# Kernel optimization log

Measured on AMD Instinct MI355X. Metric: run time of the kernel, lower is better.

## Reference

```python
import jax, jax.numpy as jnp
import numpy as np

B, C, H, W = 16, 256, 64, 64
C8, C2 = C // 8, C // 2


def conv1x1(x, w, b):
    # x: [B,Cin,H,W], w: [Cout,Cin], b: [Cout]
    return jnp.einsum('oc,bchw->bohw', w, x) + b[None, :, None, None]


def maxpool2(x):
    # 2x2 max pool, stride 2. x: [B,C,H,W] -> [B,C,H//2,W//2]
    b, c, h, w = x.shape
    return x.reshape(b, c, h // 2, 2, w // 2, 2).max(axis=(3, 5))


def setup_inputs() -> dict:
    key = jax.random.key(0)
    ks = jax.random.split(key, 9)
    s = lambda fan_in: 1.0 / np.sqrt(fan_in)
    return {
        'x': jax.random.normal(ks[0], (B, C, H, W), jnp.float32),
        'w_theta': jax.random.normal(ks[1], (C8, C), jnp.float32) * s(C),
        'b_theta': jax.random.normal(ks[2], (C8,), jnp.float32) * 0.01,
        'w_phi': jax.random.normal(ks[3], (C8, C), jnp.float32) * s(C),
        'b_phi': jax.random.normal(ks[4], (C8,), jnp.float32) * 0.01,
        'w_g': jax.random.normal(ks[5], (C2, C), jnp.float32) * s(C),
        'b_g': jax.random.normal(ks[6], (C2,), jnp.float32) * 0.01,
        'w_o': jax.random.normal(ks[7], (C, C2), jnp.float32) * s(C2),
        'b_o': jax.random.normal(ks[8], (C,), jnp.float32) * 0.01,
        'gamma': jnp.full((1,), 0.5, jnp.float32),
    }


def reference(x, w_theta, b_theta, w_phi, b_phi, w_g, b_g, w_o, b_o, gamma):
    b, c, h, w = x.shape
    n, m = h * w, (h * w) // 4
    theta = conv1x1(x, w_theta, b_theta).reshape(b, C8, n)        # [B,C/8,N]
    phi = maxpool2(conv1x1(x, w_phi, b_phi)).reshape(b, C8, m)    # [B,C/8,M]
    g = maxpool2(conv1x1(x, w_g, b_g)).reshape(b, C2, m)          # [B,C/2,M]
    # beta = softmax(theta^T phi) over keys M
    scores = jnp.einsum('bcn,bcm->bnm', theta, phi)               # [B,N,M]
    beta = jax.nn.softmax(scores, axis=-1)
    o_pre = jnp.einsum('bcm,bnm->bcn', g, beta).reshape(b, C2, h, w)
    o = conv1x1(o_pre, w_o, b_o)                                  # [B,C,H,W]
    return gamma[0] * o + x
```

## Files before the change

kernel.cpp:

```cpp
#include <hip/hip_runtime.h>
#include <hip/hip_bf16.h>

#define BB 16
#define NN 4096
#define MM 1024

typedef __attribute__((ext_vector_type(8))) short bf16x8;
typedef __attribute__((ext_vector_type(4))) float f32x4;

__device__ __forceinline__ unsigned short f2bfbits(float f) {
    union { float f; unsigned u; } v; v.f = f;
    unsigned r = v.u + 0x7fffu + ((v.u >> 16) & 1u);
    return (unsigned short)(r >> 16);
}
__device__ __forceinline__ float bfraw(unsigned short u) {
    union { unsigned u; float f; } v; v.u = ((unsigned)u) << 16; return v.f;
}

__global__ void prep_kernel(
    const float* __restrict__ wt, const float* __restrict__ bt,
    const float* __restrict__ wp, const float* __restrict__ bp,
    const float* __restrict__ wg, const float* __restrict__ bg,
    const float* __restrict__ wo,
    unsigned short* __restrict__ w_all, unsigned short* __restrict__ w_o_bf,
    float* __restrict__ b_all)
{
    int i = blockIdx.x * 256 + threadIdx.x;
    if (i < 8192)        w_all[i] = f2bfbits(wt[i]);
    else if (i < 16384)  w_all[i] = f2bfbits(wp[i - 8192]);
    else if (i < 49152)  w_all[i] = f2bfbits(wg[i - 16384]);
    else if (i < 81920)  w_o_bf[i - 49152] = f2bfbits(wo[i - 49152]);
    else if (i < 82112) {
        int r = i - 81920;
        b_all[r] = (r < 32) ? bt[r] : (r < 64) ? bp[r - 32] : bg[r - 64];
    }
}

__global__ __launch_bounds__(256, 2) void proj_kernel(
    const float* __restrict__ x,
    const unsigned short* __restrict__ w_all,
    const float* __restrict__ b_all,
    unsigned short* __restrict__ theta_t,
    unsigned short* __restrict__ phi_t,
    unsigned short* __restrict__ g)
{
    __shared__ unsigned short ot[192 * 136];

    const int t = threadIdx.x;
    const int w = t >> 6;
    const int l = t & 63;
    const int lr = l & 15, lg = l >> 4;
    const int b  = blockIdx.x >> 5;
    const int pt = blockIdx.x & 31;
    const int pbase = pt << 7;
    const int mb = pt << 5;

    f32x4 acc[3][8];
    #pragma unroll
    for (int i = 0; i < 3; ++i)
        #pragma unroll
        for (int nt = 0; nt < 8; ++nt) acc[i][nt] = (f32x4){0.f,0.f,0.f,0.f};

    const float* xb = x + (size_t)b * 256 * 4096 + pbase + lr;

    #pragma unroll 1
    for (int ks = 0; ks < 8; ++ks) {
        bf16x8 af[3];
        #pragma unroll
        for (int i = 0; i < 3; ++i)
            af[i] = *(const bf16x8*)(w_all + (size_t)(16*(3*w+i) + lr)*256 + 32*ks + 8*lg);
        #pragma unroll
        for (int nt = 0; nt < 8; ++nt) {
            const float* xp = xb + 16*nt + (size_t)(32*ks + 8*lg) * 4096;
            union { bf16x8 v; unsigned short u[8]; } bx;
            #pragma unroll
            for (int j = 0; j < 8; ++j) bx.u[j] = f2bfbits(xp[(size_t)j * 4096]);
            #pragma unroll
            for (int i = 0; i < 3; ++i)
                acc[i][nt] = __builtin_amdgcn_mfma_f32_16x16x32_bf16(af[i], bx.v, acc[i][nt], 0, 0, 0);
        }
    }

    float bias[3][4];
    #pragma unroll
    for (int i = 0; i < 3; ++i)
        #pragma unroll
        for (int r = 0; r < 4; ++r) bias[i][r] = b_all[16*(3*w+i) + 4*lg + r];
    #pragma unroll
    for (int i = 0; i < 3; ++i)
        #pragma unroll
        for (int nt = 0; nt < 8; ++nt)
            #pragma unroll
            for (int r = 0; r < 4; ++r)
                ot[(16*(3*w+i) + 4*lg + r)*136 + 16*nt + lr] =
                    f2bfbits(acc[i][nt][r] + bias[i][r]);
    __syncthreads();

    if (t < 128) {
        int p = t;
        union { unsigned short u[32]; int4 v[4]; } th;
        #pragma unroll
        for (int c = 0; c < 32; ++c) th.u[c] = ot[c*136 + p];
        int4* dst = (int4*)(theta_t + ((size_t)(b*4096 + pbase + p)) * 32);
        #pragma unroll
        for (int q = 0; q < 4; ++q) dst[q] = th.v[q];
    }
    {
        int ww = t >> 3, c0 = (t & 7) * 4;
        union { unsigned short u[4]; int2 v; } ph;
        #pragma unroll
        for (int e = 0; e < 4; ++e) {
            int row = 32 + c0 + e;
            unsigned p01 = *(const unsigned*)&ot[row*136 + 2*ww];
            unsigned p23 = *(const unsigned*)&ot[row*136 + 64 + 2*ww];
            float m0 = fmaxf(bfraw((unsigned short)p01), bfraw((unsigned short)(p01 >> 16)));
            float m1 = fmaxf(bfraw((unsigned short)p23), bfraw((unsigned short)(p23 >> 16)));
            ph.u[e] = f2bfbits(fmaxf(m0, m1));
        }
        *(int2*)(phi_t + ((size_t)(b*1024 + mb + ww)) * 32 + c0) = ph.v;
    }
    {
        int c2 = t >> 1, w0 = (t & 1) * 16;
        int row = 64 + c2;
        union { unsigned short u[16]; int4 v[2]; } gv;
        #pragma unroll
        for (int e = 0; e < 16; ++e) {
            int ww = w0 + e;
            unsigned p01 = *(const unsigned*)&ot[row*136 + 2*ww];
            unsigned p23 = *(const unsigned*)&ot[row*136 + 64 + 2*ww];
            float m0 = fmaxf(bfraw((unsigned short)p01), bfraw((unsigned short)(p01 >> 16)));
            float m1 = fmaxf(bfraw((unsigned short)p23), bfraw((unsigned short)(p23 >> 16)));
            gv.u[e] = f2bfbits(fmaxf(m0, m1));
        }
        int4* dst = (int4*)(g + ((size_t)(b*128 + c2)) * 1024 + mb + w0);
        dst[0] = gv.v[0]; dst[1] = gv.v[1];
    }
}

__global__ __launch_bounds__(64, 2) void attn_kernel(
    const unsigned short* __restrict__ theta_t,
    const unsigned short* __restrict__ phi_t,
    const unsigned short* __restrict__ g,
    unsigned short* __restrict__ o_pre_t)
{
    __shared__ unsigned short plds[32 * 72];
    __shared__ unsigned short olds[32 * 136];

    const int l = threadIdx.x;
    const int lr = l & 15, lg = l >> 4;
    const int b  = blockIdx.x >> 7;
    const int nb = (blockIdx.x & 127) << 5;

    const f32x4 zero = {0.f, 0.f, 0.f, 0.f};

    bf16x8 aq[2];
    #pragma unroll
    for (int qt = 0; qt < 2; ++qt)
        aq[qt] = *(const bf16x8*)(theta_t + ((size_t)(b*4096 + nb + 16*qt + lr))*32 + 8*lg);

    f32x4 po[2][8];
    #pragma unroll
    for (int qt = 0; qt < 2; ++qt)
        #pragma unroll
        for (int ct = 0; ct < 8; ++ct) po[qt][ct] = zero;
    float mr[2][4], lrun[2][4];
    #pragma unroll
    for (int qt = 0; qt < 2; ++qt)
        #pragma unroll
        for (int r = 0; r < 4; ++r) { mr[qt][r] = -1e30f; lrun[qt][r] = 0.f; }

    const unsigned short* phb = phi_t + (size_t)b * 1024 * 32;
    const unsigned short* gb  = g + (size_t)b * 128 * 1024;

    #pragma unroll 1
    for (int kt = 0; kt < 16; ++kt) {
        const int mb = kt * 64;
        f32x4 s[2][4];
        #pragma unroll
        for (int mt = 0; mt < 4; ++mt) {
            bf16x8 bp = *(const bf16x8*)(phb + (size_t)(mb + 16*mt + lr)*32 + 8*lg);
            s[0][mt] = __builtin_amdgcn_mfma_f32_16x16x32_bf16(aq[0], bp, zero, 0, 0, 0);
            s[1][mt] = __builtin_amdgcn_mfma_f32_16x16x32_bf16(aq[1], bp, zero, 0, 0, 0);
        }
        float sc[2][4];
        #pragma unroll
        for (int qt = 0; qt < 2; ++qt)
            #pragma unroll
            for (int r = 0; r < 4; ++r) {
                float mx = fmaxf(fmaxf(s[qt][0][r], s[qt][1][r]),
                                 fmaxf(s[qt][2][r], s[qt][3][r]));
                #pragma unroll
                for (int msk = 1; msk < 16; msk <<= 1) mx = fmaxf(mx, __shfl_xor(mx, msk));
                float nm  = fmaxf(mr[qt][r], mx);
                float scv = __expf(mr[qt][r] - nm);
                mr[qt][r] = nm; sc[qt][r] = scv;
                float ls = 0.f;
                #pragma unroll
                for (int mt = 0; mt < 4; ++mt) {
                    float p = __expf(s[qt][mt][r] - nm);
                    s[qt][mt][r] = p; ls += p;
                }
                #pragma unroll
                for (int msk = 1; msk < 16; msk <<= 1) ls += __shfl_xor(ls, msk);
                lrun[qt][r] = lrun[qt][r] * scv + ls;
            }
        #pragma unroll
        for (int qt = 0; qt < 2; ++qt)
            #pragma unroll
            for (int ct = 0; ct < 8; ++ct)
                #pragma unroll
                for (int r = 0; r < 4; ++r) po[qt][ct][r] *= sc[qt][r];
        #pragma unroll
        for (int qt = 0; qt < 2; ++qt)
            #pragma unroll
            for (int mt = 0; mt < 4; ++mt)
                #pragma unroll
                for (int r = 0; r < 4; ++r)
                    plds[(16*qt + 4*lg + r)*72 + 16*mt + lr] = f2bfbits(s[qt][mt][r]);
        #pragma unroll
        for (int ks = 0; ks < 2; ++ks) {
            bf16x8 pa0 = *(const bf16x8*)(plds + (size_t)lr*72 + 32*ks + 8*lg);
            bf16x8 pa1 = *(const bf16x8*)(plds + (size_t)(16 + lr)*72 + 32*ks + 8*lg);
            #pragma unroll
            for (int ct = 0; ct < 8; ++ct) {
                bf16x8 bg = *(const bf16x8*)(gb + (size_t)(16*ct + lr)*1024 + mb + 32*ks + 8*lg);
                po[0][ct] = __builtin_amdgcn_mfma_f32_16x16x32_bf16(pa0, bg, po[0][ct], 0, 0, 0);
                po[1][ct] = __builtin_amdgcn_mfma_f32_16x16x32_bf16(pa1, bg, po[1][ct], 0, 0, 0);
            }
        }
    }

    float inv[2][4];
    #pragma unroll
    for (int qt = 0; qt < 2; ++qt)
        #pragma unroll
        for (int r = 0; r < 4; ++r) inv[qt][r] = 1.f / lrun[qt][r];
    #pragma unroll
    for (int qt = 0; qt < 2; ++qt)
        #pragma unroll
        for (int ct = 0; ct < 8; ++ct)
            #pragma unroll
            for (int r = 0; r < 4; ++r)
                olds[(16*qt + 4*lg + r)*136 + 16*ct + lr] =
                    f2bfbits(po[qt][ct][r] * inv[qt][r]);
    #pragma unroll
    for (int i = 0; i < 8; ++i) {
        int idx = i * 64 + l;
        int q = idx >> 4, ch = idx & 15;
        int4 v = *(const int4*)(olds + q*136 + 8*ch);
        *(int4*)(o_pre_t + ((size_t)(b*4096 + nb + q))*128 + 8*ch) = v;
    }
}

__global__ __launch_bounds__(256, 2) void out_kernel(
    const unsigned short* __restrict__ o_pre_t,
    const unsigned short* __restrict__ w_o_bf,
    const float* __restrict__ b_o,
    const float* __restrict__ x,
    const float* __restrict__ gamma,
    float* __restrict__ out)
{
    const int t = threadIdx.x;
    const int w = t >> 6, l = t & 63;
    const int lr = l & 15, lg = l >> 4;
    const int b   = blockIdx.x >> 6;
    const int nbv = (blockIdx.x & 63) << 6;

    f32x4 acc[4][4];
    #pragma unroll
    for (int i = 0; i < 4; ++i)
        #pragma unroll
        for (int nt = 0; nt < 4; ++nt) acc[i][nt] = (f32x4){0.f,0.f,0.f,0.f};

    #pragma unroll 1
    for (int ks = 0; ks < 4; ++ks) {
        bf16x8 aw[4], bo[4];
        #pragma unroll
        for (int i = 0; i < 4; ++i)
            aw[i] = *(const bf16x8*)(w_o_bf + (size_t)(16*(4*w+i) + lr)*128 + 32*ks + 8*lg);
        #pragma unroll
        for (int nt = 0; nt < 4; ++nt)
            bo[nt] = *(const bf16x8*)(o_pre_t + ((size_t)(b*4096 + nbv + 16*nt + lr))*128 + 32*ks + 8*lg);
        #pragma unroll
        for (int i = 0; i < 4; ++i)
            #pragma unroll
            for (int nt = 0; nt < 4; ++nt)
                acc[i][nt] = __builtin_amdgcn_mfma_f32_16x16x32_bf16(aw[i], bo[nt], acc[i][nt], 0, 0, 0);
    }

    const float gam = gamma[0];
    float bias[4][4];
    #pragma unroll
    for (int i = 0; i < 4; ++i)
        #pragma unroll
        for (int r = 0; r < 4; ++r) bias[i][r] = b_o[16*(4*w+i) + 4*lg + r];

    #pragma unroll
    for (int i = 0; i < 4; ++i)
        #pragma unroll
        for (int nt = 0; nt < 4; ++nt)
            #pragma unroll
            for (int r = 0; r < 4; ++r) {
                int co = 16*(4*w+i) + 4*lg + r;
                int n  = nbv + 16*nt + lr;
                size_t off = ((size_t)(b*256 + co)) * 4096 + n;
                out[off] = gam * (acc[i][nt][r] + bias[i][r]) + x[off];
            }
}

extern "C" void kernel_launch(void* const* d_in, const int* in_sizes, int n_in,
                              void* d_out, int out_size, void* d_ws, size_t ws_size,
                              hipStream_t stream)
{
    const float* x       = (const float*)d_in[0];
    const float* w_theta = (const float*)d_in[1];
    const float* b_theta = (const float*)d_in[2];
    const float* w_phi   = (const float*)d_in[3];
    const float* b_phi   = (const float*)d_in[4];
    const float* w_g     = (const float*)d_in[5];
    const float* b_g     = (const float*)d_in[6];
    const float* w_o     = (const float*)d_in[7];
    const float* b_o     = (const float*)d_in[8];
    const float* gamma   = (const float*)d_in[9];
    float* outp = (float*)d_out;

    char* ws = (char*)d_ws;
    unsigned short* w_all   = (unsigned short*)ws;
    unsigned short* w_o_bf  = (unsigned short*)(ws + 98304);
    float*          b_all   = (float*)(ws + 163840);
    unsigned short* theta_t = (unsigned short*)(ws + (1u << 20));
    unsigned short* phi_t   = (unsigned short*)(ws + (5u << 20));
    unsigned short* g       = (unsigned short*)(ws + (6u << 20));
    unsigned short* o_pre_t = (unsigned short*)(ws + (10u << 20));

    prep_kernel<<<321, 256, 0, stream>>>(w_theta, b_theta, w_phi, b_phi,
                                         w_g, b_g, w_o, w_all, w_o_bf, b_all);
    proj_kernel<<<BB * 32, 256, 0, stream>>>(x, w_all, b_all, theta_t, phi_t, g);
    attn_kernel<<<BB * 128, 64, 0, stream>>>(theta_t, phi_t, g, o_pre_t);
    out_kernel<<<BB * 64, 256, 0, stream>>>(o_pre_t, w_o_bf, b_o, x, gamma, outp);
}
```

Measured before the change: 293.2 us.

## Pre-transpose x to bf16 channel-last and restructure attention to one query tile per wave

Adds a kernel that converts x to bf16 in a [B,N,C] layout so the projection kernel loads contiguous bf16x8 fragments instead of eight strided fp32 loads per fragment. The attention kernel is reorganised so each wave handles 16 queries, with 4 waves per 256-thread block. Scores are computed transposed (phi as A operand), which lets the softmax reductions use two cross-group shuffles instead of four-step butterflies. This costs an extra pass over x and more workspace, and x_t aliases o_pre_t because their lifetimes do not overlap.

```diff
diff --git a/kernel.cpp b/kernel.cpp
--- a/kernel.cpp
+++ b/kernel.cpp
@@ -2,8 +2,6 @@
 #include <hip/hip_bf16.h>
 
 #define BB 16
-#define NN 4096
-#define MM 1024
 
 typedef __attribute__((ext_vector_type(8))) short bf16x8;
 typedef __attribute__((ext_vector_type(4))) float f32x4;
@@ -15,6 +13,9 @@
 }
 __device__ __forceinline__ float bfraw(unsigned short u) {
     union { unsigned u; float f; } v; v.u = ((unsigned)u) << 16; return v.f;
+}
+__device__ __forceinline__ unsigned packbf2(float lo, float hi) {
+    return (unsigned)f2bfbits(lo) | ((unsigned)f2bfbits(hi) << 16);
 }
 
 __global__ void prep_kernel(
@@ -36,8 +37,44 @@
     }
 }
 
+__global__ __launch_bounds__(256) void xt_kernel(
+    const float* __restrict__ x, unsigned short* __restrict__ x_t)
+{
+    __shared__ unsigned short lt[64 * 74];
+
+    const int t = threadIdx.x;
+    const int bid = blockIdx.x;
+    const int b  = bid >> 8;
+    const int p0 = ((bid >> 2) & 63) << 6;
+    const int c0 = (bid & 3) << 6;
+
+    {
+        int c = t & 63, seg = t >> 6;
+        const float* src = x + ((size_t)(b * 256 + c0 + c)) * 4096 + p0 + seg * 16;
+        #pragma unroll
+        for (int j = 0; j < 4; ++j) {
+            float4 v = *(const float4*)(src + 4 * j);
+            unsigned* dst = (unsigned*)(lt + c * 74 + seg * 16 + 4 * j);
+            dst[0] = packbf2(v.x, v.y);
+            dst[1] = packbf2(v.z, v.w);
+        }
+    }
+    __syncthreads();
+    {
+        int p = t >> 2, quad = t & 3;
+        #pragma unroll
+        for (int h = 0; h < 2; ++h) {
+            union { unsigned short u[8]; int4 v; } o;
+            #pragma unroll
+            for (int e = 0; e < 8; ++e)
+                o.u[e] = lt[(quad * 16 + h * 8 + e) * 74 + p];
+            *(int4*)(x_t + ((size_t)(b * 4096 + p0 + p)) * 256 + c0 + quad * 16 + h * 8) = o.v;
+        }
+    }
+}
+
 __global__ __launch_bounds__(256, 2) void proj_kernel(
-    const float* __restrict__ x,
+    const unsigned short* __restrict__ x_t,
     const unsigned short* __restrict__ w_all,
     const float* __restrict__ b_all,
     unsigned short* __restrict__ theta_t,
@@ -61,8 +98,6 @@
         #pragma unroll
         for (int nt = 0; nt < 8; ++nt) acc[i][nt] = (f32x4){0.f,0.f,0.f,0.f};
 
-    const float* xb = x + (size_t)b * 256 * 4096 + pbase + lr;
-
     #pragma unroll 1
     for (int ks = 0; ks < 8; ++ks) {
         bf16x8 af[3];
@@ -71,13 +106,10 @@
             af[i] = *(const bf16x8*)(w_all + (size_t)(16*(3*w+i) + lr)*256 + 32*ks + 8*lg);
         #pragma unroll
         for (int nt = 0; nt < 8; ++nt) {
-            const float* xp = xb + 16*nt + (size_t)(32*ks + 8*lg) * 4096;
-            union { bf16x8 v; unsigned short u[8]; } bx;
-            #pragma unroll
-            for (int j = 0; j < 8; ++j) bx.u[j] = f2bfbits(xp[(size_t)j * 4096]);
+            bf16x8 bx = *(const bf16x8*)(x_t + ((size_t)(b*4096 + pbase + 16*nt + lr))*256 + 32*ks + 8*lg);
             #pragma unroll
             for (int i = 0; i < 3; ++i)
-                acc[i][nt] = __builtin_amdgcn_mfma_f32_16x16x32_bf16(af[i], bx.v, acc[i][nt], 0, 0, 0);
+                acc[i][nt] = __builtin_amdgcn_mfma_f32_16x16x32_bf16(af[i], bx, acc[i][nt], 0, 0, 0);
         }
     }
 
@@ -137,118 +169,104 @@
     }
 }
 
-__global__ __launch_bounds__(64, 2) void attn_kernel(
+__global__ __launch_bounds__(256, 4) void attn_kernel(
     const unsigned short* __restrict__ theta_t,
     const unsigned short* __restrict__ phi_t,
     const unsigned short* __restrict__ g,
     unsigned short* __restrict__ o_pre_t)
 {
-    __shared__ unsigned short plds[32 * 72];
-    __shared__ unsigned short olds[32 * 136];
-
-    const int l = threadIdx.x;
+    __shared__ unsigned short plds[4][16 * 72];
+    __shared__ unsigned short olds[4][16 * 136];
+
+    const int t = threadIdx.x;
+    const int wv = t >> 6;
+    const int l  = t & 63;
     const int lr = l & 15, lg = l >> 4;
-    const int b  = blockIdx.x >> 7;
-    const int nb = (blockIdx.x & 127) << 5;
+    const int b   = blockIdx.x >> 6;
+    const int nq0 = (blockIdx.x & 63) * 64 + wv * 16;
 
     const f32x4 zero = {0.f, 0.f, 0.f, 0.f};
 
-    bf16x8 aq[2];
-    #pragma unroll
-    for (int qt = 0; qt < 2; ++qt)
-        aq[qt] = *(const bf16x8*)(theta_t + ((size_t)(b*4096 + nb + 16*qt + lr))*32 + 8*lg);
-
-    f32x4 po[2][8];
-    #pragma unroll
-    for (int qt = 0; qt < 2; ++qt)
-        #pragma unroll
-        for (int ct = 0; ct < 8; ++ct) po[qt][ct] = zero;
-    float mr[2][4], lrun[2][4];
-    #pragma unroll
-    for (int qt = 0; qt < 2; ++qt)
-        #pragma unroll
-        for (int r = 0; r < 4; ++r) { mr[qt][r] = -1e30f; lrun[qt][r] = 0.f; }
+    const bf16x8 aq = *(const bf16x8*)(theta_t + ((size_t)(b*4096 + nq0 + lr))*32 + 8*lg);
+
+    f32x4 po[8];
+    #pragma unroll
+    for (int ct = 0; ct < 8; ++ct) po[ct] = zero;
+    float m_run = -1e30f, l_run = 0.f;
 
     const unsigned short* phb = phi_t + (size_t)b * 1024 * 32;
     const unsigned short* gb  = g + (size_t)b * 128 * 1024;
+    unsigned short* pw = plds[wv];
 
     #pragma unroll 1
     for (int kt = 0; kt < 16; ++kt) {
         const int mb = kt * 64;
-        f32x4 s[2][4];
+        f32x4 s[4];
         #pragma unroll
         for (int mt = 0; mt < 4; ++mt) {
-            bf16x8 bp = *(const bf16x8*)(phb + (size_t)(mb + 16*mt + lr)*32 + 8*lg);
-            s[0][mt] = __builtin_amdgcn_mfma_f32_16x16x32_bf16(aq[0], bp, zero, 0, 0, 0);
-            s[1][mt] = __builtin_amdgcn_mfma_f32_16x16x32_bf16(aq[1], bp, zero, 0, 0, 0);
-        }
-        float sc[2][4];
-        #pragma unroll
-        for (int qt = 0; qt < 2; ++qt)
+            bf16x8 ap = *(const bf16x8*)(phb + (size_t)(mb + 16*mt + lr)*32 + 8*lg);
+            s[mt] = __builtin_amdgcn_mfma_f32_16x16x32_bf16(ap, aq, zero, 0, 0, 0);
+        }
+        float mx = -1e30f;
+        #pragma unroll
+        for (int mt = 0; mt < 4; ++mt)
+            #pragma unroll
+            for (int r = 0; r < 4; ++r) mx = fmaxf(mx, s[mt][r]);
+        mx = fmaxf(mx, __shfl_xor(mx, 16));
+        mx = fmaxf(mx, __shfl_xor(mx, 32));
+        float nm = fmaxf(m_run, mx);
+        float sc = __expf(m_run - nm);
+        float ls = 0.f;
+        #pragma unroll
+        for (int mt = 0; mt < 4; ++mt)
             #pragma unroll
             for (int r = 0; r < 4; ++r) {
-                float mx = fmaxf(fmaxf(s[qt][0][r], s[qt][1][r]),
-                                 fmaxf(s[qt][2][r], s[qt][3][r]));
-                #pragma unroll
-                for (int msk = 1; msk < 16; msk <<= 1) mx = fmaxf(mx, __shfl_xor(mx, msk));
-                float nm  = fmaxf(mr[qt][r], mx);
-                float scv = __expf(mr[qt][r] - nm);
-                mr[qt][r] = nm; sc[qt][r] = scv;
-                float ls = 0.f;
-                #pragma unroll
-                for (int mt = 0; mt < 4; ++mt) {
-                    float p = __expf(s[qt][mt][r] - nm);
-                    s[qt][mt][r] = p; ls += p;
-                }
-                #pragma unroll
-                for (int msk = 1; msk < 16; msk <<= 1) ls += __shfl_xor(ls, msk);
-                lrun[qt][r] = lrun[qt][r] * scv + ls;
+                float p = __expf(s[mt][r] - nm);
+                s[mt][r] = p; ls += p;
             }
-        #pragma unroll
-        for (int qt = 0; qt < 2; ++qt)
-            #pragma unroll
-            for (int ct = 0; ct < 8; ++ct)
-                #pragma unroll
-                for (int r = 0; r < 4; ++r) po[qt][ct][r] *= sc[qt][r];
-        #pragma unroll
-        for (int qt = 0; qt < 2; ++qt)
-            #pragma unroll
-            for (int mt = 0; mt < 4; ++mt)
-                #pragma unroll
-                for (int r = 0; r < 4; ++r)
-                    plds[(16*qt + 4*lg + r)*72 + 16*mt + lr] = f2bfbits(s[qt][mt][r]);
+        ls += __shfl_xor(ls, 16);
+        ls += __shfl_xor(ls, 32);
+        l_run = l_run * sc + ls;
+        m_run = nm;
+        float scB[4];
+        #pragma unroll
+        for (int r = 0; r < 4; ++r) scB[r] = __shfl(sc, 4*lg + r);
+        #pragma unroll
+        for (int ct = 0; ct < 8; ++ct)
+            #pragma unroll
+            for (int r = 0; r < 4; ++r) po[ct][r] *= scB[r];
+        #pragma unroll
+        for (int mt = 0; mt < 4; ++mt)
+            #pragma unroll
+            for (int i = 0; i < 2; ++i)
+                *(unsigned*)(pw + lr*72 + 16*mt + 4*lg + 2*i) =
+                    packbf2(s[mt][2*i], s[mt][2*i + 1]);
         #pragma unroll
         for (int ks = 0; ks < 2; ++ks) {
-            bf16x8 pa0 = *(const bf16x8*)(plds + (size_t)lr*72 + 32*ks + 8*lg);
-            bf16x8 pa1 = *(const bf16x8*)(plds + (size_t)(16 + lr)*72 + 32*ks + 8*lg);
+            bf16x8 pa = *(const bf16x8*)(pw + lr*72 + 32*ks + 8*lg);
             #pragma unroll
             for (int ct = 0; ct < 8; ++ct) {
-                bf16x8 bg = *(const bf16x8*)(gb + (size_t)(16*ct + lr)*1024 + mb + 32*ks + 8*lg);
-                po[0][ct] = __builtin_amdgcn_mfma_f32_16x16x32_bf16(pa0, bg, po[0][ct], 0, 0, 0);
-                po[1][ct] = __builtin_amdgcn_mfma_f32_16x16x32_bf16(pa1, bg, po[1][ct], 0, 0, 0);
+                bf16x8 bgv = *(const bf16x8*)(gb + (size_t)(16*ct + lr)*1024 + mb + 32*ks + 8*lg);
+                po[ct] = __builtin_amdgcn_mfma_f32_16x16x32_bf16(pa, bgv, po[ct], 0, 0, 0);
             }
         }
     }
 
-    float inv[2][4];
-    #pragma unroll
-    for (int qt = 0; qt < 2; ++qt)
-        #pragma unroll
-        for (int r = 0; r < 4; ++r) inv[qt][r] = 1.f / lrun[qt][r];
-    #pragma unroll
-    for (int qt = 0; qt < 2; ++qt)
-        #pragma unroll
-        for (int ct = 0; ct < 8; ++ct)
-            #pragma unroll
-            for (int r = 0; r < 4; ++r)
-                olds[(16*qt + 4*lg + r)*136 + 16*ct + lr] =
-                    f2bfbits(po[qt][ct][r] * inv[qt][r]);
-    #pragma unroll
-    for (int i = 0; i < 8; ++i) {
-        int idx = i * 64 + l;
-        int q = idx >> 4, ch = idx & 15;
-        int4 v = *(const int4*)(olds + q*136 + 8*ch);
-        *(int4*)(o_pre_t + ((size_t)(b*4096 + nb + q))*128 + 8*ch) = v;
+    float invq = 1.f / l_run;
+    float invB[4];
+    #pragma unroll
+    for (int r = 0; r < 4; ++r) invB[r] = __shfl(invq, 4*lg + r);
+    unsigned short* ow = olds[wv];
+    #pragma unroll
+    for (int ct = 0; ct < 8; ++ct)
+        #pragma unroll
+        for (int r = 0; r < 4; ++r)
+            ow[(4*lg + r)*136 + 16*ct + lr] = f2bfbits(po[ct][r] * invB[r]);
+    #pragma unroll
+    for (int i = 0; i < 4; ++i) {
+        int q = 4*i + lg;
+        int4 v = *(const int4*)(ow + q*136 + 8*lr);
+        *(int4*)(o_pre_t + ((size_t)(b*4096 + nq0 + q))*128 + 8*lr) = v;
     }
 }
 
@@ -328,14 +346,16 @@
     unsigned short* w_all   = (unsigned short*)ws;
     unsigned short* w_o_bf  = (unsigned short*)(ws + 98304);
     float*          b_all   = (float*)(ws + 163840);
-    unsigned short* theta_t = (unsigned short*)(ws + (1u << 20));
-    unsigned short* phi_t   = (unsigned short*)(ws + (5u << 20));
-    unsigned short* g       = (unsigned short*)(ws + (6u << 20));
-    unsigned short* o_pre_t = (unsigned short*)(ws + (10u << 20));
+    unsigned short* x_t     = (unsigned short*)(ws + (1u << 20));
+    unsigned short* o_pre_t = (unsigned short*)(ws + (1u << 20));
+    unsigned short* theta_t = (unsigned short*)(ws + (33u << 20));
+    unsigned short* phi_t   = (unsigned short*)(ws + (37u << 20));
+    unsigned short* g       = (unsigned short*)(ws + (38u << 20));
 
     prep_kernel<<<321, 256, 0, stream>>>(w_theta, b_theta, w_phi, b_phi,
                                          w_g, b_g, w_o, w_all, w_o_bf, b_all);
-    proj_kernel<<<BB * 32, 256, 0, stream>>>(x, w_all, b_all, theta_t, phi_t, g);
-    attn_kernel<<<BB * 128, 64, 0, stream>>>(theta_t, phi_t, g, o_pre_t);
+    xt_kernel<<<BB * 256, 256, 0, stream>>>(x, x_t);
+    proj_kernel<<<BB * 32, 256, 0, stream>>>(x_t, w_all, b_all, theta_t, phi_t, g);
+    attn_kernel<<<BB * 64, 256, 0, stream>>>(theta_t, phi_t, g, o_pre_t);
     out_kernel<<<BB * 64, 256, 0, stream>>>(o_pre_t, w_o_bf, b_o, x, gamma, outp);
 }
```

New measurement: 315.1 us. +7.5%, slower.
